# Kernel optimization log

Hardware: AMD Instinct MI355X
Metric: run time of the kernel (lower is better)

The kernel has to match this reference:

```python
import jax, jax.numpy as jnp
import numpy as np

N_QUBITS = 8
INPUT_DIM = 128
HIDDEN = 8
T = 512
B = 512


def _build_circuit_consts(n):
    # wire 0 is the most-significant bit of the 2^n basis index (torchquantum layout)
    dim = 1 << n
    idx = np.arange(dim)
    bits = (idx[:, None] >> (n - 1 - np.arange(n))) & 1          # [dim, n]
    zsign = (1 - 2 * bits).astype(np.float32)                     # <Z_w> signs, [dim, n]
    # compose CNOT(0,1)...CNOT(n-2,n-1), CNOT(n-1,0) into one permutation
    perm = idx.copy()
    pairs = [(i, i + 1) for i in range(n - 1)] + [(n - 1, 0)]
    for c, t in pairs:
        cmask = 1 << (n - 1 - c)
        tmask = 1 << (n - 1 - t)
        g = np.where(idx & cmask, idx ^ tmask, idx)               # flip target bit if control set
        perm = perm[g]
    return jnp.asarray(perm), jnp.asarray(zsign)

_PERM, _ZSIGN = _build_circuit_consts(N_QUBITS)


def _qlayer(z, theta):
    # RX(x) then RX(theta) on |0> per wire -> product state; CNOT ring permutes the
    # basis amplitudes, so probabilities permute; MeasureAll(PauliZ) = probs @ zsign.
    a = 0.5 * (z + theta[None, :])                                # [B, n]
    pq = jnp.stack([jnp.cos(a) ** 2, jnp.sin(a) ** 2], axis=-1)   # [B, n, 2]
    probs = pq[:, 0, :]
    for w in range(1, N_QUBITS):                                  # small fixed kron loop
        probs = (probs[:, :, None] * pq[:, w, None, :]).reshape(probs.shape[0], -1)
    probs = probs[:, _PERM]                                       # CNOT ring
    return probs @ _ZSIGN                                         # [B, n] expvals in [-1, 1]


def setup_inputs() -> dict:
    key = jax.random.key(0)
    ks = jax.random.split(key, 14)
    d_in = INPUT_DIM + HIDDEN
    mk_w = lambda k: jax.random.normal(k, (d_in, N_QUBITS), dtype=jnp.float32) * 0.05
    mk_t = lambda k: jax.random.normal(k, (N_QUBITS,), dtype=jnp.float32) * 0.1
    return {
        "inputs": jax.random.normal(ks[0], (T, B, INPUT_DIM), dtype=jnp.float32),
        "Wf": mk_w(ks[1]), "bf": jnp.zeros((N_QUBITS,), jnp.float32),
        "Wi": mk_w(ks[2]), "bi": jnp.zeros((N_QUBITS,), jnp.float32),
        "Wu": mk_w(ks[3]), "bu": jnp.zeros((N_QUBITS,), jnp.float32),
        "Wo": mk_w(ks[4]), "bo": jnp.zeros((N_QUBITS,), jnp.float32),
        "theta_f": mk_t(ks[5]), "theta_i": mk_t(ks[6]),
        "theta_u": mk_t(ks[7]), "theta_o": mk_t(ks[8]),
    }


def reference(inputs, Wf, bf, Wi, bi, Wu, bu, Wo, bo,
              theta_f, theta_i, theta_u, theta_o):
    hx0 = jnp.zeros((inputs.shape[1], HIDDEN), inputs.dtype)
    cx0 = jnp.zeros((inputs.shape[1], HIDDEN), inputs.dtype)

    def step(carry, x):
        hx, cx = carry
        comb = jnp.concatenate([x, hx], axis=1)                   # [B, D+H]
        f = jax.nn.sigmoid(_qlayer(comb @ Wf + bf, theta_f))
        i = jax.nn.sigmoid(_qlayer(comb @ Wi + bi, theta_i))
        g = jnp.tanh(_qlayer(comb @ Wu + bu, theta_u))
        o = jax.nn.sigmoid(_qlayer(comb @ Wo + bo, theta_o))
        cx = f * cx + i * g
        hx = o * jnp.tanh(cx)
        return (hx, cx), hx

    (hx, cx), outputs = jax.lax.scan(step, (hx0, cx0), inputs)
    return outputs, hx, cx
```

## Files before the change

kernel.cpp:

```cpp
#include <hip/hip_runtime.h>
#include <stdint.h>

#define T_STEPS 512
#define BATCH   512
#define IN_DIM  128
#define GDIM    32
#define SLICE   (BATCH * GDIM)
#define INV2PI  0.15915494309189535f

typedef float f4 __attribute__((ext_vector_type(4)));

template <int CTRL>
__device__ __forceinline__ float dppm(float x) {
    return __int_as_float(__builtin_amdgcn_mov_dpp(__float_as_int(x), CTRL, 0xF, 0xF, true));
}
template <int CTRL>
__device__ __forceinline__ float dppk(float old, float x) {
    return __int_as_float(__builtin_amdgcn_update_dpp(
        __float_as_int(old), __float_as_int(x), CTRL, 0xF, 0xF, false));
}

__device__ __forceinline__ float tanh_pade(float x) {
    float u = x * x;
    float n = fmaf(u, u + 105.0f, 945.0f);
    float d = fmaf(u, fmaf(u, 15.0f, 420.0f), 945.0f);
    return (x * n) * __builtin_amdgcn_rcpf(d);
}

__device__ __forceinline__ void gload_lds16(const float* g, float* l) {
    __builtin_amdgcn_global_load_lds(
        (const __attribute__((address_space(1))) void*)g,
        (__attribute__((address_space(3))) void*)l, 16, 0, 0);
}

__global__ __launch_bounds__(512) void qlstm_xproj(
    const float* __restrict__ inp,
    const float* __restrict__ Wf, const float* __restrict__ bf,
    const float* __restrict__ Wi, const float* __restrict__ bi,
    const float* __restrict__ Wu, const float* __restrict__ bu,
    const float* __restrict__ Wo, const float* __restrict__ bo,
    const float* __restrict__ thf, const float* __restrict__ thi,
    const float* __restrict__ thu, const float* __restrict__ tho,
    float* __restrict__ X)
{
    __shared__ float tile[2][64 * 130];
    const int tid = threadIdx.x;
    const int t0  = blockIdx.x * 8;
    const bool producer = (tid < 256);

    if (producer) {
        const f4* src = (const f4*)(inp + (long long)t0 * 64 * IN_DIM);
        #pragma unroll
        for (int j = 0; j < 8; ++j) {
            int f = tid + j * 256;
            f4 v = __builtin_nontemporal_load(src + f);
            int r = f >> 5, c = (f & 31) << 2;
            float* d = &tile[0][r * 130 + c];
            d[0] = v.x; d[1] = v.y; d[2] = v.z; d[3] = v.w;
        }
    }

    const int c0 = tid - 256;
    const int g  = __builtin_amdgcn_readfirstlane(c0 >> 6) & 3;
    const int rl = c0 & 63;
    const float* W  = (g == 0) ? Wf : (g == 1) ? Wi : (g == 2) ? Wu : Wo;
    const float* B  = (g == 0) ? bf : (g == 1) ? bi : (g == 2) ? bu : bo;
    const float* TH = (g == 0) ? thf : (g == 1) ? thi : (g == 2) ? thu : tho;
    float binit[8];
    #pragma unroll
    for (int j = 0; j < 8; ++j) binit[j] = B[j] + TH[j];

    __syncthreads();

    for (int i = 0; i < 8; ++i) {
        if (producer) {
            if (i < 7) {
                const f4* src = (const f4*)(inp + (long long)(t0 + i + 1) * 64 * IN_DIM);
                f4 v[8];
                #pragma unroll
                for (int j = 0; j < 8; ++j)
                    v[j] = __builtin_nontemporal_load(src + tid + j * 256);
                float* buf = tile[(i + 1) & 1];
                #pragma unroll
                for (int j = 0; j < 8; ++j) {
                    int f = tid + j * 256;
                    int r = f >> 5, c = (f & 31) << 2;
                    float* d = &buf[r * 130 + c];
                    d[0] = v[j].x; d[1] = v[j].y; d[2] = v[j].z; d[3] = v[j].w;
                }
            }
        } else {
            float acc[8];
            #pragma unroll
            for (int j = 0; j < 8; ++j) acc[j] = binit[j];

            const float2* trow = (const float2*)&tile[i & 1][rl * 130];
            #pragma unroll 8
            for (int k2 = 0; k2 < 64; ++k2) {
                float2 v = trow[k2];
                int k = 2 * k2;
                #pragma unroll
                for (int j = 0; j < 8; ++j) {
                    acc[j] = fmaf(v.x, W[k * 8 + j], acc[j]);
                    acc[j] = fmaf(v.y, W[(k + 1) * 8 + j], acc[j]);
                }
            }

            long long row0 = (long long)(t0 + i) * 64;
            float4* Xo = (float4*)(X + (row0 + rl) * GDIM + g * 8);
            Xo[0] = make_float4(acc[0] * INV2PI, acc[1] * INV2PI, acc[2] * INV2PI, acc[3] * INV2PI);
            Xo[1] = make_float4(acc[4] * INV2PI, acc[5] * INV2PI, acc[6] * INV2PI, acc[7] * INV2PI);
        }
        __syncthreads();
    }
}

__global__ __launch_bounds__(64, 1) void qlstm_rec(
    const float* __restrict__ X,
    const float* __restrict__ Wf, const float* __restrict__ Wi,
    const float* __restrict__ Wu, const float* __restrict__ Wo,
    float* __restrict__ out)
{
    __shared__ float xb[2 * 2 * 128 * 32];

    const int lane = threadIdx.x;
    const int p    = lane & 15;
    const int q    = p >> 1;
    const int par  = lane & 1;
    const int s    = lane >> 5;
    const int bb   = (lane >> 4) & 1;
    const int qd   = (lane >> 2) & 3;
    const int gate = s * 2 + par;
    const int b    = blockIdx.x * 2 + bb;
    const int col  = s * 16 + par * 8 + q;

    const bool isq0   = (q == 0);
    const bool loHalf = (lane < 32);
    const bool sB     = (s == 1);
    const bool parB   = (par == 1);

    const float* Wg = (gate == 0) ? Wf : (gate == 1) ? Wi : (gate == 2) ? Wu : Wo;
    float wv[8];
    #pragma unroll
    for (int i = 0; i < 8; ++i)
        wv[i] = Wg[(IN_DIM + (i ^ (qd << 1))) * 8 + q] * INV2PI;

    const bool  isT = (gate == 2);
    const float G0 = isT ? 0.9999014f  : 0.24997535f;
    const float G1 = isT ? -0.3310474f : -0.02069046f;
    const float G2 = isT ? 0.1204402f  : 0.00188188f;
    const float G3 = isT ? -0.0277f    : -0.000108203f;
    const float bbv = isT ? 0.0f : 0.5f;

    const float* g0 = X + (lane >> 3) * SLICE + (lane & 7) * 4
                        + blockIdx.x * 2 * GDIM;
    auto stage = [&](int bi, int qs) {
        #pragma unroll
        for (int j = 0; j < 2; ++j) {
            float* dst = &xb[(bi * 2 + j) * 4096];
            const float* srcb = g0 + j * GDIM + qs * SLICE;
            #pragma unroll
            for (int n = 0; n < 16; ++n)
                gload_lds16(srcb + n * 8 * SLICE, dst + n * 256);
        }
    };

    stage(0, 0);
    asm volatile("s_waitcnt vmcnt(0)" ::: "memory");

    const float* xq0 = &xb[bb * 4096 + col];
    float xv0 = xq0[0];
    float xv1 = xq0[32];
    stage(1, 128);

    float hx = 0.0f, cx = 0.0f;
    const float ONE = 1.0f;
    float* outp = out + b * 8 + q;

    for (int qt = 0; qt < 4; ++qt) {
        const int bi = qt & 1;
        const float* xq = &xb[bi * 8192 + bb * 4096 + col];
        if (qt > 0) {
            asm volatile("s_waitcnt vmcnt(0)" ::: "memory");
            xv0 = xq[0];
            xv1 = xq[32];
            if (qt < 3) stage(1 - bi, (qt + 1) * 128);
        }

        auto qstep = [&](int t, int ls, float& XV) {
            float xv = XV;
            XV = xq[((ls + 2) & 127) * 32];

            float Ba = dppm<0x00>(hx);
            float Bb = dppm<0xAA>(hx);
            float Bc = dppm<0x141>(Ba);
            float Bd = dppm<0x141>(Bb);
            float Be = dppm<0x140>(Ba);
            float Bf = dppm<0x140>(Bb);
            float Bg = dppm<0x128>(Ba);
            float Bk = dppm<0x128>(Bb);

            float A1 = fmaf(Bb, wv[1], fmaf(Ba, wv[0], xv));
            float A2 = fmaf(Bd, wv[3], Bc * wv[2]);
            float A3 = fmaf(Bf, wv[7], Be * wv[6]);
            float A4 = fmaf(Bk, wv[5], Bg * wv[4]);
            float z  = (A1 + A2) + (A3 + A4);

            float cq = __builtin_amdgcn_cosf(z);

            float cc  = fabsf(cq) < 1e-30f ? 1e-30f : cq;
            float rcpc = __builtin_amdgcn_rcpf(cc);

            float P = cq * dppk<0x112>(ONE, cq);
            P = P * dppk<0x114>(ONE, P);
            P = P * dppk<0x118>(ONE, P);

            float Pfull = dppm<0x10E>(P);
            float out0  = Pfull * rcpc;
            float outv  = isq0 ? out0 : P;

            float u  = outv * outv;
            float u2 = u * u;
            float t1 = fmaf(u, G1, G0);
            float t2 = fmaf(u, G3, G2);
            float G  = fmaf(u2, t2, t1);
            float act = fmaf(outv, G, bbv);

            float n1 = dppm<0xB1>(act);
            auto pr = __builtin_amdgcn_permlane32_swap(
                __float_as_int(act), __float_as_int(act), false, false);
            float sw = __int_as_float(loHalf ? pr[1] : pr[0]);
            float sw2 = dppm<0xB1>(sw);

            float X1 = parB ? n1  : act;
            float X2 = parB ? act : n1;
            float Y1 = parB ? sw2 : sw;
            float Y2 = parB ? sw  : sw2;

            float fv = sB ? Y1 : X1;
            float iv = sB ? Y2 : X2;
            float uv = sB ? X1 : Y1;
            float ov = sB ? X2 : Y2;

            float ncx = fmaf(fv, cx, iv * uv);
            float nhx = ov * tanh_pade(ncx);
            cx = ncx;
            hx = nhx;

            __builtin_nontemporal_store(nhx, outp + t * (BATCH * 8));
        };

        #pragma unroll 2
        for (int ls = 0; ls < 128; ls += 2) {
            qstep(qt * 128 + ls,     ls,     xv0);
            qstep(qt * 128 + ls + 1, ls + 1, xv1);
        }
    }

    __builtin_nontemporal_store(hx, out + T_STEPS * BATCH * 8 + b * 8 + q);
    __builtin_nontemporal_store(cx, out + T_STEPS * BATCH * 8 + (BATCH + b) * 8 + q);
}

extern "C" void kernel_launch(void* const* d_in, const int* in_sizes, int n_in,
                              void* d_out, int out_size, void* d_ws, size_t ws_size,
                              hipStream_t stream) {
    const float* inp = (const float*)d_in[0];
    const float* Wf  = (const float*)d_in[1];
    const float* bf  = (const float*)d_in[2];
    const float* Wi  = (const float*)d_in[3];
    const float* bi  = (const float*)d_in[4];
    const float* Wu  = (const float*)d_in[5];
    const float* bu  = (const float*)d_in[6];
    const float* Wo  = (const float*)d_in[7];
    const float* bo  = (const float*)d_in[8];
    const float* thf = (const float*)d_in[9];
    const float* thi = (const float*)d_in[10];
    const float* thu = (const float*)d_in[11];
    const float* tho = (const float*)d_in[12];

    float* X   = (float*)d_ws;
    float* out = (float*)d_out;

    qlstm_xproj<<<(T_STEPS * BATCH) / (64 * 8), 512, 0, stream>>>(
        inp, Wf, bf, Wi, bi, Wu, bu, Wo, bo, thf, thi, thu, tho, X);

    qlstm_rec<<<BATCH / 2, 64, 0, stream>>>(X, Wf, Wi, Wu, Wo, out);
}
```

Measured before the change: 125.5 us.

## Split input projection into one 64-row block per workgroup with K halves

```diff
diff --git a/kernel.cpp b/kernel.cpp
--- a/kernel.cpp
+++ b/kernel.cpp
@@ -43,20 +43,27 @@
     const float* __restrict__ thu, const float* __restrict__ tho,
     float* __restrict__ X)
 {
-    __shared__ float tile[2][64 * 130];
+    __shared__ float tile[2][64 * 66];
     const int tid = threadIdx.x;
-    const int t0  = blockIdx.x * 8;
+    const long long row0 = (long long)blockIdx.x * 64;
     const bool producer = (tid < 256);
 
+    f4 v0[4], v1[4];
     if (producer) {
-        const f4* src = (const f4*)(inp + (long long)t0 * 64 * IN_DIM);
-        #pragma unroll
-        for (int j = 0; j < 8; ++j) {
+        #pragma unroll
+        for (int j = 0; j < 4; ++j) {
             int f = tid + j * 256;
-            f4 v = __builtin_nontemporal_load(src + f);
-            int r = f >> 5, c = (f & 31) << 2;
-            float* d = &tile[0][r * 130 + c];
-            d[0] = v.x; d[1] = v.y; d[2] = v.z; d[3] = v.w;
+            int r = f >> 4, c16 = f & 15;
+            const float* rb = inp + (row0 + r) * IN_DIM;
+            v0[j] = __builtin_nontemporal_load((const f4*)rb + c16);
+            v1[j] = __builtin_nontemporal_load((const f4*)(rb + 64) + c16);
+        }
+        #pragma unroll
+        for (int j = 0; j < 4; ++j) {
+            int f = tid + j * 256;
+            int r = f >> 4, c16 = f & 15;
+            float* d = &tile[0][r * 66 + c16 * 4];
+            d[0] = v0[j].x; d[1] = v0[j].y; d[2] = v0[j].z; d[3] = v0[j].w;
         }
     }
 
@@ -66,52 +73,53 @@
     const float* W  = (g == 0) ? Wf : (g == 1) ? Wi : (g == 2) ? Wu : Wo;
     const float* B  = (g == 0) ? bf : (g == 1) ? bi : (g == 2) ? bu : bo;
     const float* TH = (g == 0) ? thf : (g == 1) ? thi : (g == 2) ? thu : tho;
-    float binit[8];
+
+    float acc[8];
     #pragma unroll
-    for (int j = 0; j < 8; ++j) binit[j] = B[j] + TH[j];
+    for (int j = 0; j < 8; ++j) acc[j] = B[j] + TH[j];
 
     __syncthreads();
 
-    for (int i = 0; i < 8; ++i) {
-        if (producer) {
-            if (i < 7) {
-                const f4* src = (const f4*)(inp + (long long)(t0 + i + 1) * 64 * IN_DIM);
-                f4 v[8];
-                #pragma unroll
-                for (int j = 0; j < 8; ++j)
-                    v[j] = __builtin_nontemporal_load(src + tid + j * 256);
-                float* buf = tile[(i + 1) & 1];
-                #pragma unroll
-                for (int j = 0; j < 8; ++j) {
-                    int f = tid + j * 256;
-                    int r = f >> 5, c = (f & 31) << 2;
-                    float* d = &buf[r * 130 + c];
-                    d[0] = v[j].x; d[1] = v[j].y; d[2] = v[j].z; d[3] = v[j].w;
-                }
+    if (producer) {
+        #pragma unroll
+        for (int j = 0; j < 4; ++j) {
+            int f = tid + j * 256;
+            int r = f >> 4, c16 = f & 15;
+            float* d = &tile[1][r * 66 + c16 * 4];
+            d[0] = v1[j].x; d[1] = v1[j].y; d[2] = v1[j].z; d[3] = v1[j].w;
+        }
+    } else {
+        const float2* trow = (const float2*)&tile[0][rl * 66];
+        #pragma unroll 8
+        for (int k2 = 0; k2 < 32; ++k2) {
+            float2 v = trow[k2];
+            int k = 2 * k2;
+            #pragma unroll
+            for (int j = 0; j < 8; ++j) {
+                acc[j] = fmaf(v.x, W[k * 8 + j], acc[j]);
+                acc[j] = fmaf(v.y, W[(k + 1) * 8 + j], acc[j]);
             }
-        } else {
-            float acc[8];
+        }
+    }
+
+    __syncthreads();
+
+    if (!producer) {
+        const float2* trow = (const float2*)&tile[1][rl * 66];
+        #pragma unroll 8
+        for (int k2 = 0; k2 < 32; ++k2) {
+            float2 v = trow[k2];
+            int k = 64 + 2 * k2;
             #pragma unroll
-            for (int j = 0; j < 8; ++j) acc[j] = binit[j];
-
-            const float2* trow = (const float2*)&tile[i & 1][rl * 130];
-            #pragma unroll 8
-            for (int k2 = 0; k2 < 64; ++k2) {
-                float2 v = trow[k2];
-                int k = 2 * k2;
-                #pragma unroll
-                for (int j = 0; j < 8; ++j) {
-                    acc[j] = fmaf(v.x, W[k * 8 + j], acc[j]);
-                    acc[j] = fmaf(v.y, W[(k + 1) * 8 + j], acc[j]);
-                }
+            for (int j = 0; j < 8; ++j) {
+                acc[j] = fmaf(v.x, W[k * 8 + j], acc[j]);
+                acc[j] = fmaf(v.y, W[(k + 1) * 8 + j], acc[j]);
             }
-
-            long long row0 = (long long)(t0 + i) * 64;
-            float4* Xo = (float4*)(X + (row0 + rl) * GDIM + g * 8);
-            Xo[0] = make_float4(acc[0] * INV2PI, acc[1] * INV2PI, acc[2] * INV2PI, acc[3] * INV2PI);
-            Xo[1] = make_float4(acc[4] * INV2PI, acc[5] * INV2PI, acc[6] * INV2PI, acc[7] * INV2PI);
-        }
-        __syncthreads();
+        }
+
+        float4* Xo = (float4*)(X + (row0 + rl) * GDIM + g * 8);
+        Xo[0] = make_float4(acc[0] * INV2PI, acc[1] * INV2PI, acc[2] * INV2PI, acc[3] * INV2PI);
+        Xo[1] = make_float4(acc[4] * INV2PI, acc[5] * INV2PI, acc[6] * INV2PI, acc[7] * INV2PI);
     }
 }
 
@@ -281,7 +289,7 @@
     float* X   = (float*)d_ws;
     float* out = (float*)d_out;
 
-    qlstm_xproj<<<(T_STEPS * BATCH) / (64 * 8), 512, 0, stream>>>(
+    qlstm_xproj<<<(T_STEPS * BATCH) / 64, 512, 0, stream>>>(
         inp, Wf, bf, Wi, bi, Wu, bu, Wo, bo, thf, thi, thu, tho, X);
 
     qlstm_rec<<<BATCH / 2, 64, 0, stream>>>(X, Wf, Wi, Wu, Wo, out);
```

Result: no change. 126.4 us (+0.7%).
